# Optimization experiments

Hardware: AMD Instinct MI355X
Metric: run time of the kernel (lower is better)

The kernel has to match this reference:

```python
import jax, jax.numpy as jnp
import numpy as np

N = 50000
E = 800000
F_IN = 128
HID = 32
HEADS = 4
NCLS = 16
NEG_SLOPE = 0.2


def setup_inputs() -> dict:
    key = jax.random.key(0)
    ks = jax.random.split(key, 10)
    x = jax.random.normal(ks[0], (N, F_IN), dtype=jnp.float32)
    edge_index = jax.random.randint(ks[1], (2, E), 0, N, dtype=jnp.int32)
    W1 = jax.random.normal(ks[2], (F_IN, HEADS * HID), dtype=jnp.float32) * 0.1
    a_src1 = jax.random.normal(ks[3], (HEADS, HID), dtype=jnp.float32) * 0.1
    a_dst1 = jax.random.normal(ks[4], (HEADS, HID), dtype=jnp.float32) * 0.1
    b1 = jax.random.normal(ks[5], (HEADS * HID,), dtype=jnp.float32) * 0.1
    W2 = jax.random.normal(ks[6], (HEADS * HID, NCLS), dtype=jnp.float32) * 0.1
    a_src2 = jax.random.normal(ks[7], (1, NCLS), dtype=jnp.float32) * 0.1
    a_dst2 = jax.random.normal(ks[8], (1, NCLS), dtype=jnp.float32) * 0.1
    b2 = jax.random.normal(ks[9], (NCLS,), dtype=jnp.float32) * 0.1
    return {"x": x, "edge_index": edge_index, "W1": W1, "a_src1": a_src1,
            "a_dst1": a_dst1, "b1": b1, "W2": W2, "a_src2": a_src2,
            "a_dst2": a_dst2, "b2": b2}


def _gat_layer(x, src, dst, W, a_src, a_dst, bias, heads, out_dim, concat):
    n = x.shape[0]
    h = (x @ W).reshape(n, heads, out_dim)               # [N,H,D]
    al_s = jnp.einsum('nhd,hd->nh', h, a_src)            # [N,H]
    al_d = jnp.einsum('nhd,hd->nh', h, a_dst)            # [N,H]
    e = jax.nn.leaky_relu(al_s[src] + al_d[dst], NEG_SLOPE)  # [E,H]
    # segment softmax over destination nodes
    m = jax.ops.segment_max(e, dst, num_segments=n)      # [N,H]
    ex = jnp.exp(e - m[dst])                             # [E,H]
    den = jax.ops.segment_sum(ex, dst, num_segments=n)   # [N,H]
    alpha = ex / den[dst]
    msg = h[src] * alpha[:, :, None]                     # [E,H,D]
    out = jax.ops.segment_sum(msg, dst, num_segments=n)  # [N,H,D]
    if concat:
        out = out.reshape(n, heads * out_dim)
    else:
        out = out.mean(axis=1)
    return out + bias


def reference(x, edge_index, W1, a_src1, a_dst1, b1, W2, a_src2, a_dst2, b2):
    # PyG GATConv default add_self_loops=True
    loops = jnp.arange(N, dtype=edge_index.dtype)
    src = jnp.concatenate([edge_index[0], loops])
    dst = jnp.concatenate([edge_index[1], loops])
    h = _gat_layer(x, src, dst, W1, a_src1, a_dst1, b1, HEADS, HID, True)
    h = jax.nn.elu(h)
    out = _gat_layer(h, src, dst, W2, a_src2, a_dst2, b2, 1, NCLS, False)
    return jax.nn.log_softmax(out, axis=1)
```

## Files before the change

### kernel.cpp

```cpp
#include <hip/hip_runtime.h>
#include <hip/hip_bf16.h>

#define N_NODES 50000
#define N_EDGES 800000
#define ET (N_EDGES + N_NODES)
#define F_IN 128
#define HH 128
#define HEADS 4
#define HID 32
#define NCLS 16
#define NEG 0.2f
#define CAP 96
#define CSTR 16

#define GB ((N_NODES + 63) / 64)
#define FBX ((ET + 1023) / 1024)

typedef unsigned short u16;
typedef short bf16x8 __attribute__((ext_vector_type(8)));
typedef float f32x4 __attribute__((ext_vector_type(4)));
typedef u16 u16x8 __attribute__((ext_vector_type(8)));

__device__ __forceinline__ float lrelu(float x) { return x > 0.f ? x : NEG * x; }
__device__ __forceinline__ float bu2f(u16 u) { return __uint_as_float(((unsigned)u) << 16); }
__device__ __forceinline__ u16 f2bu(float f) {
    __hip_bfloat16 h = __float2bfloat16(f);
    return *reinterpret_cast<u16*>(&h);
}

__device__ __forceinline__ void edge_sd(const int* __restrict__ ei, int i, int& s, int& d) {
    if (i < N_EDGES) { s = ei[i]; d = ei[N_EDGES + i]; }
    else             { s = i - N_EDGES; d = s; }
}

__global__ void __launch_bounds__(256) k_fill_gemm1(
        const int* __restrict__ ei, int* __restrict__ cnt, u16* __restrict__ esrc,
        const float* __restrict__ x, const float* __restrict__ W1,
        const float* __restrict__ a_s, const float* __restrict__ a_d,
        u16* __restrict__ h1b, float* __restrict__ al_s, float* __restrict__ al_d) {
    __shared__ u16 w1t[128 * 136];
    int bid = blockIdx.x;
    bool is_gemm = ((bid & 1) == 0) && ((bid >> 1) < GB);
    if (!is_gemm) {
        int fid = bid - min((bid + 1) >> 1, GB);
        int base = fid * 1024 + threadIdx.x;
        int s[4], d[4], pos[4];
        bool v[4];
#pragma unroll
        for (int k = 0; k < 4; ++k) {
            int i = base + k * 256;
            v[k] = i < ET;
            if (v[k]) edge_sd(ei, i, s[k], d[k]);
        }
#pragma unroll
        for (int k = 0; k < 4; ++k)
            if (v[k]) pos[k] = atomicAdd(&cnt[d[k] * CSTR], 1);
#pragma unroll
        for (int k = 0; k < 4; ++k)
            if (v[k] && pos[k] < CAP) esrc[d[k] * CAP + pos[k]] = (u16)s[k];
        return;
    }
    int q = bid >> 1;
    int t = threadIdx.x;
    for (int it = 0; it < 64; ++it) {
        int idx = it * 256 + t;
        int k = idx >> 7, n = idx & 127;
        w1t[n * 136 + k] = f2bu(W1[idx]);
    }
    __syncthreads();
    int wave = t >> 6, lane = t & 63;
    int col = lane & 15, quad = lane >> 4;
    int tb = q * 64 + wave * 16;
    union { bf16x8 v; u16 u[8]; } af[4];
    int anode = tb + col;
    bool aval = anode < N_NODES;
    const float* xr = x + (size_t)anode * F_IN + quad * 8;
#pragma unroll
    for (int kb = 0; kb < 4; ++kb) {
        float4 lo = aval ? ((const float4*)(xr + kb * 32))[0] : make_float4(0.f, 0.f, 0.f, 0.f);
        float4 hi = aval ? ((const float4*)(xr + kb * 32))[1] : make_float4(0.f, 0.f, 0.f, 0.f);
        af[kb].u[0] = f2bu(lo.x); af[kb].u[1] = f2bu(lo.y);
        af[kb].u[2] = f2bu(lo.z); af[kb].u[3] = f2bu(lo.w);
        af[kb].u[4] = f2bu(hi.x); af[kb].u[5] = f2bu(hi.y);
        af[kb].u[6] = f2bu(hi.z); af[kb].u[7] = f2bu(hi.w);
    }
    float ps[4][4] = {}, pd[4][4] = {};
#pragma unroll
    for (int nt = 0; nt < 8; ++nt) {
        f32x4 acc = {0.f, 0.f, 0.f, 0.f};
#pragma unroll
        for (int kb = 0; kb < 4; ++kb) {
            bf16x8 bf = *(const bf16x8*)&w1t[(nt * 16 + col) * 136 + kb * 32 + quad * 8];
            acc = __builtin_amdgcn_mfma_f32_16x16x32_bf16(af[kb].v, bf, acc, 0, 0, 0);
        }
        int feat = nt * 16 + col;
        float asv = a_s[feat], adv = a_d[feat];
        const int head = nt >> 1;
#pragma unroll
        for (int rr = 0; rr < 4; ++rr) {
            int node = tb + quad * 4 + rr;
            float v = acc[rr];
            if (node < N_NODES) h1b[(size_t)node * HH + feat] = f2bu(v);
            ps[rr][head] = fmaf(v, asv, ps[rr][head]);
            pd[rr][head] = fmaf(v, adv, pd[rr][head]);
        }
    }
#pragma unroll
    for (int rr = 0; rr < 4; ++rr)
#pragma unroll
        for (int h = 0; h < 4; ++h)
#pragma unroll
            for (int w = 1; w < 16; w <<= 1) {
                ps[rr][h] += __shfl_xor(ps[rr][h], w);
                pd[rr][h] += __shfl_xor(pd[rr][h], w);
            }
    if (col == 0) {
#pragma unroll
        for (int rr = 0; rr < 4; ++rr) {
            int node = tb + quad * 4 + rr;
            if (node < N_NODES) {
#pragma unroll
                for (int h = 0; h < 4; ++h) {
                    al_s[node * 4 + h] = ps[rr][h];
                    al_d[node * 4 + h] = pd[rr][h];
                }
            }
        }
    }
}

__global__ void __launch_bounds__(256) k_agg1(
        const u16* __restrict__ esrc, const int* __restrict__ cnt,
        const float* __restrict__ alS, const float* __restrict__ alD,
        const u16* __restrict__ h1b, const float* __restrict__ b1,
        const float* __restrict__ W2, const float* __restrict__ a_s2,
        const float* __restrict__ a_d2,
        u16* __restrict__ h2b, float* __restrict__ alS2, float* __restrict__ alD2) {
    __shared__ float wls[4][CAP * HEADS];
    __shared__ int   sls[4][CAP];
    __shared__ __align__(16) float rowf[4][HH];
    __shared__ float w2t[NCLS * 132];
    __shared__ float as2s[NCLS], ad2s[NCLS];
    int t = threadIdx.x;
    for (int idx = t; idx < F_IN * NCLS; idx += 256) {
        int f = idx >> 4, c = idx & 15;
        w2t[c * 132 + f] = W2[idx];
    }
    if (t < NCLS) { as2s[t] = a_s2[t]; ad2s[t] = a_d2[t]; }
    __syncthreads();
    int wave = t >> 6, lane = t & 63;
    int n = blockIdx.x * 4 + wave;
    int off = n * CAP;
    int deg = min(cnt[n * CSTR], CAP);
    int dm1 = deg - 1;
    int sreg = (int)esrc[off + min(lane, dm1)];
    if (lane < deg) sls[wave][lane] = sreg;
    for (int e = 64 + lane; e < deg; e += 64)
        sls[wave][e] = (int)esrc[off + e];
    int quarter = lane >> 4, fl = lane & 15;
    int hb = fl >> 2;
    u16x8 qf[6];
#pragma unroll
    for (int d = 0; d < 6; ++d) {
        int sp = __shfl(sreg, min(quarter + 4 * d, dm1));
        qf[d] = ((const u16x8*)(h1b + (size_t)sp * HH))[fl];
    }
    int slot = lane & 15, h = lane >> 4;
    int s0 = __shfl(sreg, min(slot, dm1));
    int s1 = __shfl(sreg, min(slot + 16, dm1));
    float av0 = alS[(size_t)s0 * 4 + h];
    float av1 = alS[(size_t)s1 * 4 + h];
    float ad = alD[n * 4 + h];
    float den = 0.f;
    if (slot < deg) {
        float wv = __expf(lrelu(av0 + ad));
        wls[wave][slot * 4 + h] = wv; den += wv;
    }
    if (slot + 16 < deg) {
        float wv = __expf(lrelu(av1 + ad));
        wls[wave][(slot + 16) * 4 + h] = wv; den += wv;
    }
    for (int e = slot + 32; e < deg; e += 16) {
        int s = (int)esrc[off + e];
        float av = alS[(size_t)s * 4 + h];
        float wv = __expf(lrelu(av + ad));
        wls[wave][e * 4 + h] = wv; den += wv;
    }
#pragma unroll
    for (int w = 1; w < 16; w <<= 1) den += __shfl_xor(den, w);
    float inv = 1.f / den;
    float invh = __shfl(inv, hb << 4);
    float acc[8] = {};
#pragma unroll
    for (int d = 0; d < 6; ++d) {
        int e = quarter + 4 * d;
        if (e < deg) {
            float a = wls[wave][e * 4 + hb] * invh;
#pragma unroll
            for (int j = 0; j < 8; ++j)
                acc[j] = fmaf(bu2f(qf[d][j]), a, acc[j]);
        }
    }
    for (int e = quarter + 24; e < deg; e += 4) {
        int sp = sls[wave][e];
        float a = wls[wave][e * 4 + hb] * invh;
        u16x8 qq = ((const u16x8*)(h1b + (size_t)sp * HH))[fl];
#pragma unroll
        for (int j = 0; j < 8; ++j)
            acc[j] = fmaf(bu2f(qq[j]), a, acc[j]);
    }
#pragma unroll
    for (int j = 0; j < 8; ++j) {
        acc[j] += __shfl_xor(acc[j], 16);
        acc[j] += __shfl_xor(acc[j], 32);
    }
    if (quarter == 0) {
        const float4* b4 = (const float4*)b1;
        float4 blo = b4[fl * 2], bhi = b4[fl * 2 + 1];
        float v[8];
        v[0] = acc[0] + blo.x; v[1] = acc[1] + blo.y;
        v[2] = acc[2] + blo.z; v[3] = acc[3] + blo.w;
        v[4] = acc[4] + bhi.x; v[5] = acc[5] + bhi.y;
        v[6] = acc[6] + bhi.z; v[7] = acc[7] + bhi.w;
#pragma unroll
        for (int j = 0; j < 8; ++j) v[j] = v[j] > 0.f ? v[j] : __expf(v[j]) - 1.f;
        ((float4*)&rowf[wave][0])[fl * 2]     = make_float4(v[0], v[1], v[2], v[3]);
        ((float4*)&rowf[wave][0])[fl * 2 + 1] = make_float4(v[4], v[5], v[6], v[7]);
    }
    int c = lane & 15, qq2 = lane >> 4;
    float h2acc = 0.f;
#pragma unroll
    for (int i = 0; i < 32; ++i) {
        int f = i * 4 + qq2;
        h2acc = fmaf(rowf[wave][f], w2t[c * 132 + f], h2acc);
    }
    h2acc += __shfl_xor(h2acc, 16);
    h2acc += __shfl_xor(h2acc, 32);
    if (lane < 16) h2b[(size_t)n * NCLS + lane] = f2bu(h2acc);
    float rs = h2acc * as2s[c], rd = h2acc * ad2s[c];
#pragma unroll
    for (int w = 1; w < 16; w <<= 1) { rs += __shfl_xor(rs, w); rd += __shfl_xor(rd, w); }
    if (lane == 0) { alS2[n] = rs; alD2[n] = rd; }
}

__global__ void __launch_bounds__(256) k_agg2(
        const u16* __restrict__ esrc, const int* __restrict__ cnt,
        const float* __restrict__ alS2, const float* __restrict__ alD2,
        const u16* __restrict__ h2b, const float* __restrict__ b2,
        float* __restrict__ out) {
    __shared__ float wls[4][CAP];
    __shared__ int   sls[4][CAP];
    int wave = threadIdx.x >> 6, lane = threadIdx.x & 63;
    int n = blockIdx.x * 4 + wave;
    int off = n * CAP;
    int deg = min(cnt[n * CSTR], CAP);
    int dm1 = deg - 1;
    int sub = lane >> 3, cp = lane & 7;
    int sreg = (int)esrc[off + min(lane, dm1)];
    unsigned qf[4];
#pragma unroll
    for (int d = 0; d < 4; ++d) {
        int sp = __shfl(sreg, min(sub + 8 * d, dm1));
        qf[d] = ((const unsigned*)(h2b + (size_t)sp * NCLS))[cp];
    }
    float av = alS2[sreg];
    float ad = alD2[n];
    float den = 0.f;
    float wv = __expf(lrelu(av + ad));
    if (lane < deg) { wls[wave][lane] = wv; sls[wave][lane] = sreg; den = wv; }
    for (int e = 64 + lane; e < deg; e += 64) {
        int s = (int)esrc[off + e];
        float a2 = alS2[s];
        float w2v = __expf(lrelu(a2 + ad));
        wls[wave][e] = w2v; sls[wave][e] = s; den += w2v;
    }
#pragma unroll
    for (int w = 1; w < 64; w <<= 1) den += __shfl_xor(den, w);
    float inv = 1.f / den;
    float a0 = 0.f, a1 = 0.f;
#pragma unroll
    for (int d = 0; d < 4; ++d) {
        int e = sub + 8 * d;
        if (e < deg) {
            float al = wls[wave][e] * inv;
            a0 = fmaf(bu2f((u16)(qf[d] & 0xffffu)), al, a0);
            a1 = fmaf(bu2f((u16)(qf[d] >> 16)), al, a1);
        }
    }
    for (int e = sub + 32; e < deg; e += 8) {
        int s = sls[wave][e];
        float al = wls[wave][e] * inv;
        unsigned qq = ((const unsigned*)(h2b + (size_t)s * NCLS))[cp];
        a0 = fmaf(bu2f((u16)(qq & 0xffffu)), al, a0);
        a1 = fmaf(bu2f((u16)(qq >> 16)), al, a1);
    }
    a0 += __shfl_xor(a0, 8);  a1 += __shfl_xor(a1, 8);
    a0 += __shfl_xor(a0, 16); a1 += __shfl_xor(a1, 16);
    a0 += __shfl_xor(a0, 32); a1 += __shfl_xor(a1, 32);
    float v0 = a0 + b2[2 * cp], v1 = a1 + b2[2 * cp + 1];
    float mx = fmaxf(v0, v1);
#pragma unroll
    for (int w = 1; w < 8; w <<= 1) mx = fmaxf(mx, __shfl_xor(mx, w));
    float ex = __expf(v0 - mx) + __expf(v1 - mx);
#pragma unroll
    for (int w = 1; w < 8; w <<= 1) ex += __shfl_xor(ex, w);
    float lse = mx + __logf(ex);
    if (lane < 8) ((float2*)(out + (size_t)n * NCLS))[cp] = make_float2(v0 - lse, v1 - lse);
}

extern "C" void kernel_launch(void* const* d_in, const int* in_sizes, int n_in,
                              void* d_out, int out_size, void* d_ws, size_t ws_size,
                              hipStream_t stream) {
    const float* x   = (const float*)d_in[0];
    const int*   ei  = (const int*)d_in[1];
    const float* W1  = (const float*)d_in[2];
    const float* as1 = (const float*)d_in[3];
    const float* ad1 = (const float*)d_in[4];
    const float* b1  = (const float*)d_in[5];
    const float* W2  = (const float*)d_in[6];
    const float* as2 = (const float*)d_in[7];
    const float* ad2 = (const float*)d_in[8];
    const float* b2  = (const float*)d_in[9];
    float* out = (float*)d_out;
    char* ws = (char*)d_ws;

    u16*   h1b  = (u16*)  (ws);
    float* alS1 = (float*)(ws + 12800000);
    float* alD1 = (float*)(ws + 13600000);
    u16*   h2b  = (u16*)  (ws + 14400000);
    float* alS2 = (float*)(ws + 16000000);
    float* alD2 = (float*)(ws + 16200000);
    int*   cnt  = (int*)  (ws + 16400000);
    u16*   esrc = (u16*)  (ws + 19600000);

    hipMemsetAsync(cnt, 0, (size_t)N_NODES * CSTR * 4, stream);
    k_fill_gemm1<<<GB + FBX, 256, 0, stream>>>(ei, cnt, esrc,
                                               x, W1, as1, ad1, h1b, alS1, alD1);
    k_agg1<<<N_NODES / 4, 256, 0, stream>>>(esrc, cnt, alS1, alD1, h1b, b1,
                                            W2, as2, ad2, h2b, alS2, alD2);
    k_agg2<<<N_NODES / 4, 256, 0, stream>>>(esrc, cnt, alS2, alD2, h2b, b2, out);
}
```

Measured before the change: 198.5 us.

## Bucket edges by destination partition before per-node CSR fill

```diff
diff --git a/kernel.cpp b/kernel.cpp
--- a/kernel.cpp
+++ b/kernel.cpp
@@ -13,8 +13,12 @@
 #define CAP 96
 #define CSTR 16
 
+#define PSH 9
+#define NPART ((N_NODES + 511) >> PSH)
+#define PCAP 12288
+#define EPB 2048
+#define PB ((ET + EPB - 1) / EPB)
 #define GB ((N_NODES + 63) / 64)
-#define FBX ((ET + 1023) / 1024)
 
 typedef unsigned short u16;
 typedef short bf16x8 __attribute__((ext_vector_type(8)));
@@ -33,35 +37,63 @@
     else             { s = i - N_EDGES; d = s; }
 }
 
-__global__ void __launch_bounds__(256) k_fill_gemm1(
-        const int* __restrict__ ei, int* __restrict__ cnt, u16* __restrict__ esrc,
+__global__ void __launch_bounds__(256) k_part_gemm1(
+        const int* __restrict__ ei, int* __restrict__ pcur, unsigned* __restrict__ pbuf,
         const float* __restrict__ x, const float* __restrict__ W1,
         const float* __restrict__ a_s, const float* __restrict__ a_d,
         u16* __restrict__ h1b, float* __restrict__ al_s, float* __restrict__ al_d) {
     __shared__ u16 w1t[128 * 136];
     int bid = blockIdx.x;
-    bool is_gemm = ((bid & 1) == 0) && ((bid >> 1) < GB);
-    if (!is_gemm) {
-        int fid = bid - min((bid + 1) >> 1, GB);
-        int base = fid * 1024 + threadIdx.x;
-        int s[4], d[4], pos[4];
-        bool v[4];
-#pragma unroll
-        for (int k = 0; k < 4; ++k) {
-            int i = base + k * 256;
+    int t = threadIdx.x;
+    bool is_part = (bid < 2 * PB) && ((bid & 1) == 0);
+    if (is_part) {
+        unsigned* pcnt  = (unsigned*)w1t;
+        unsigned* pscan = pcnt + 128;
+        unsigned* gbase = pscan + 128;
+        unsigned* eb    = gbase + 128;
+        int fid = bid >> 1;
+        int base = fid * EPB;
+        int count = min(EPB, ET - base);
+        if (t < 128) pcnt[t] = 0;
+        __syncthreads();
+        int s[8], d[8], r[8], p[8];
+        bool v[8];
+#pragma unroll
+        for (int k = 0; k < 8; ++k) {
+            int i = base + k * 256 + t;
             v[k] = i < ET;
-            if (v[k]) edge_sd(ei, i, s[k], d[k]);
-        }
-#pragma unroll
-        for (int k = 0; k < 4; ++k)
-            if (v[k]) pos[k] = atomicAdd(&cnt[d[k] * CSTR], 1);
-#pragma unroll
-        for (int k = 0; k < 4; ++k)
-            if (v[k] && pos[k] < CAP) esrc[d[k] * CAP + pos[k]] = (u16)s[k];
+            if (v[k]) {
+                edge_sd(ei, i, s[k], d[k]);
+                p[k] = d[k] >> PSH;
+                r[k] = (int)atomicAdd(&pcnt[p[k]], 1u);
+            }
+        }
+        __syncthreads();
+        if (t < 128) pscan[t] = pcnt[t];
+        __syncthreads();
+        for (int st = 1; st < 128; st <<= 1) {
+            unsigned add = 0;
+            if (t < 128 && t >= st) add = pscan[t - st];
+            __syncthreads();
+            if (t < 128) pscan[t] += add;
+            __syncthreads();
+        }
+        if (t < 128) gbase[t] = pcnt[t] ? (unsigned)atomicAdd(&pcur[t * CSTR], (int)pcnt[t]) : 0u;
+        __syncthreads();
+#pragma unroll
+        for (int k = 0; k < 8; ++k)
+            if (v[k]) eb[(pscan[p[k]] - pcnt[p[k]]) + r[k]] =
+                          ((unsigned)d[k] << 16) | (unsigned)s[k];
+        __syncthreads();
+        for (int j = t; j < count; j += 256) {
+            unsigned val = eb[j];
+            int pp = (int)(val >> (16 + PSH));
+            unsigned gi = gbase[pp] + ((unsigned)j - (pscan[pp] - pcnt[pp]));
+            if (gi < PCAP) pbuf[(size_t)pp * PCAP + gi] = val;
+        }
         return;
     }
-    int q = bid >> 1;
-    int t = threadIdx.x;
+    int q = (bid < 2 * PB) ? (bid >> 1) : (bid - PB);
     for (int it = 0; it < 64; ++it) {
         int idx = it * 256 + t;
         int k = idx >> 7, n = idx & 127;
@@ -126,6 +158,20 @@
                 }
             }
         }
+    }
+}
+
+__global__ void __launch_bounds__(512) k_fill2(
+        const int* __restrict__ pcur, const unsigned* __restrict__ pbuf,
+        int* __restrict__ cnt, u16* __restrict__ esrc) {
+    int p = blockIdx.x;
+    int nE = min(pcur[p * CSTR], PCAP);
+    const unsigned* pb = pbuf + (size_t)p * PCAP;
+    for (int i = threadIdx.x; i < nE; i += 512) {
+        unsigned v = pb[i];
+        int d = (int)(v >> 16), s = (int)(v & 0xffffu);
+        int pos = atomicAdd(&cnt[d * CSTR], 1);
+        if (pos < CAP) esrc[d * CAP + pos] = (u16)s;
     }
 }
 
@@ -162,14 +208,16 @@
     u16x8 qf[6];
 #pragma unroll
     for (int d = 0; d < 6; ++d) {
-        int sp = __shfl(sreg, min(quarter + 4 * d, dm1));
-        qf[d] = ((const u16x8*)(h1b + (size_t)sp * HH))[fl];
+        int ee = quarter + 4 * d;
+        int sp = __shfl(sreg, ee);
+        if (ee < deg) qf[d] = ((const u16x8*)(h1b + (size_t)sp * HH))[fl];
     }
     int slot = lane & 15, h = lane >> 4;
-    int s0 = __shfl(sreg, min(slot, dm1));
-    int s1 = __shfl(sreg, min(slot + 16, dm1));
-    float av0 = alS[(size_t)s0 * 4 + h];
-    float av1 = alS[(size_t)s1 * 4 + h];
+    int s0 = __shfl(sreg, slot);
+    int s1 = __shfl(sreg, slot + 16);
+    float av0 = 0.f, av1 = 0.f;
+    if (slot < deg)      av0 = alS[(size_t)s0 * 4 + h];
+    if (slot + 16 < deg) av1 = alS[(size_t)s1 * 4 + h];
     float ad = alD[n * 4 + h];
     float den = 0.f;
     if (slot < deg) {
@@ -260,10 +308,12 @@
     unsigned qf[4];
 #pragma unroll
     for (int d = 0; d < 4; ++d) {
-        int sp = __shfl(sreg, min(sub + 8 * d, dm1));
-        qf[d] = ((const unsigned*)(h2b + (size_t)sp * NCLS))[cp];
-    }
-    float av = alS2[sreg];
+        int ee = sub + 8 * d;
+        int sp = __shfl(sreg, ee);
+        if (ee < deg) qf[d] = ((const unsigned*)(h2b + (size_t)sp * NCLS))[cp];
+    }
+    float av = 0.f;
+    if (lane < deg) av = alS2[sreg];
     float ad = alD2[n];
     float den = 0.f;
     float wv = __expf(lrelu(av + ad));
@@ -324,18 +374,22 @@
     float* out = (float*)d_out;
     char* ws = (char*)d_ws;
 
-    u16*   h1b  = (u16*)  (ws);
-    float* alS1 = (float*)(ws + 12800000);
-    float* alD1 = (float*)(ws + 13600000);
-    u16*   h2b  = (u16*)  (ws + 14400000);
-    float* alS2 = (float*)(ws + 16000000);
-    float* alD2 = (float*)(ws + 16200000);
-    int*   cnt  = (int*)  (ws + 16400000);
-    u16*   esrc = (u16*)  (ws + 19600000);
+    u16*      h1b  = (u16*)     (ws);
+    float*    alS1 = (float*)   (ws + 12800000);
+    float*    alD1 = (float*)   (ws + 13600000);
+    u16*      h2b  = (u16*)     (ws + 14400000);
+    float*    alS2 = (float*)   (ws + 16000000);
+    float*    alD2 = (float*)   (ws + 16200000);
+    int*      cnt  = (int*)     (ws + 16400000);
+    u16*      esrc = (u16*)     (ws + 19600000);
+    int*      pcur = (int*)     (ws + 29200000);
+    unsigned* pbuf = (unsigned*)(ws + 29220000);
 
     hipMemsetAsync(cnt, 0, (size_t)N_NODES * CSTR * 4, stream);
-    k_fill_gemm1<<<GB + FBX, 256, 0, stream>>>(ei, cnt, esrc,
-                                               x, W1, as1, ad1, h1b, alS1, alD1);
+    hipMemsetAsync(pcur, 0, (size_t)NPART * CSTR * 4, stream);
+    k_part_gemm1<<<PB + GB, 256, 0, stream>>>(ei, pcur, pbuf,
+                                              x, W1, as1, ad1, h1b, alS1, alD1);
+    k_fill2<<<NPART, 512, 0, stream>>>(pcur, pbuf, cnt, esrc);
     k_agg1<<<N_NODES / 4, 256, 0, stream>>>(esrc, cnt, alS1, alD1, h1b, b1,
                                             W2, as2, ad2, h2b, alS2, alD2);
     k_agg2<<<N_NODES / 4, 256, 0, stream>>>(esrc, cnt, alS2, alD2, h2b, b2, out);
```

Result: slower. 224.9 us (+13.3%).
